# Kernel tuning notes

Hardware: AMD Instinct MI355X
Metric: run time of the kernel (lower is better)

Reference implementation:

```python
import jax, jax.numpy as jnp
import numpy as np

EPS_BN = 1e-5
K_DET = 50

def conv2d(x, w, b, pad):
    y = jax.lax.conv_general_dilated(x, w, (1, 1), [(pad, pad), (pad, pad)],
                                     dimension_numbers=('NCHW', 'OIHW', 'NCHW'))
    return y + b[None, :, None, None]

def branch2(x, w1, b1, w2, b2):
    # conv3x3 -> relu -> conv1x1
    return conv2d(jax.nn.relu(conv2d(x, w1, b1, 1)), w2, b2, 0)

def roi_head(x, w1, b1, g, beta, m, v, w2, b2):
    # conv3x3 -> BN(eval) -> relu -> global avg pool -> conv1x1
    h = conv2d(x, w1, b1, 1)
    h = (h - m[None, :, None, None]) * (g[None, :, None, None] / jnp.sqrt(v[None, :, None, None] + EPS_BN)) + beta[None, :, None, None]
    h = jax.nn.relu(h)
    h = jnp.mean(h, axis=(2, 3), keepdims=True)
    return conv2d(h, w2, b2, 0)[:, :, 0, 0]

def nms_hm(heat, kernel=3):
    pad = (kernel - 1) // 2
    hmax = jax.lax.reduce_window(heat, -jnp.inf, jax.lax.max,
                                 (1, 1, kernel, kernel), (1, 1, 1, 1),
                                 [(0, 0), (0, 0), (pad, pad), (pad, pad)])
    return heat * (hmax == heat).astype(heat.dtype)

def select_topk(heat, K):
    B, C, H, W = heat.shape
    s_all, i_all = jax.lax.top_k(heat.reshape(B, C, H * W), K)   # per-class topk
    scores, idx = jax.lax.top_k(s_all.reshape(B, C * K), K)      # overall topk
    classes = idx // K
    inds = jnp.take_along_axis(i_all.reshape(B, C * K), idx, axis=1)  # flat HW inds
    return scores, inds, classes

def roi_align_7x7(feat, boxes, sr=2):
    # torchvision roi_align, spatial_scale=1, aligned=False, sampling_ratio=sr
    B, C, H, W = feat.shape
    N = boxes.shape[0]
    b = boxes[:, 0].astype(jnp.int32)
    x1, y1, x2, y2 = boxes[:, 1], boxes[:, 2], boxes[:, 3], boxes[:, 4]
    roi_w = jnp.maximum(x2 - x1, 1.0)
    roi_h = jnp.maximum(y2 - y1, 1.0)
    bw = roi_w / 7.0
    bh = roi_h / 7.0
    S = 7 * sr
    off = (jnp.arange(S, dtype=feat.dtype) + 0.5) / sr  # sample offsets in bin units
    xs = x1[:, None] + bw[:, None] * off[None, :]       # (N,S)
    ys = y1[:, None] + bh[:, None] * off[None, :]
    X = jnp.broadcast_to(xs[:, None, :], (N, S, S))
    Y = jnp.broadcast_to(ys[:, :, None], (N, S, S))
    valid = (X > -1.0) & (X < W) & (Y > -1.0) & (Y < H)
    Xc = jnp.clip(X, 0.0, W - 1.0)
    Yc = jnp.clip(Y, 0.0, H - 1.0)
    x0 = jnp.floor(Xc).astype(jnp.int32)
    y0 = jnp.floor(Yc).astype(jnp.int32)
    x1i = jnp.minimum(x0 + 1, W - 1)
    y1i = jnp.minimum(y0 + 1, H - 1)
    lx = Xc - x0
    ly = Yc - y0
    flat = feat.transpose(0, 2, 3, 1).reshape(B * H * W, C)
    base = (b * H * W)[:, None, None]
    g = lambda yy, xx: flat[base + yy * W + xx]  # (N,S,S,C)
    v = (((1 - ly) * (1 - lx))[..., None] * g(y0, x0)
         + ((1 - ly) * lx)[..., None] * g(y0, x1i)
         + (ly * (1 - lx))[..., None] * g(y1i, x0)
         + (ly * lx)[..., None] * g(y1i, x1i))
    v = v * valid[..., None]
    v = v.reshape(N, 7, sr, 7, sr, C).mean(axis=(2, 4))
    return v.transpose(0, 3, 1, 2)  # (N,C,7,7)

def project_to_rect(calib, pts):
    c_u, c_v = calib[:, 0, 2], calib[:, 1, 2]
    f_u, f_v = calib[:, 0, 0], calib[:, 1, 1]
    b_x = calib[:, 0, 3] / (-f_u)
    b_y = calib[:, 1, 3] / (-f_v)
    x = (pts[:, 0] - c_u) * pts[:, 2] / f_u + b_x
    y = (pts[:, 1] - c_v) * pts[:, 2] / f_v + b_y
    return jnp.stack([x, y, pts[:, 2]], -1)

HEAD_NAMES = ['dep', 'o3', 's3', 'hd']

def setup_inputs():
    key = jax.random.key(0)
    ks = iter(jax.random.split(key, 64))
    B, Cin, H, W = 8, 64, 96, 320
    HC, NC = 256, 3
    f32 = jnp.float32
    rn = lambda shape, s=0.02: s * jax.random.normal(next(ks), shape, f32)
    inp = {}
    inp['features'] = jax.random.normal(next(ks), (B, Cin, H, W), f32)
    base = jnp.array([[700., 0., 640., 0.], [0., 700., 192., 0.], [0., 0., 1., 0.]], f32)
    inp['calib'] = base[None] + (jax.random.uniform(next(ks), (B, 3, 4), f32) - 0.5) * 2.0
    crb = jnp.array([[0., 0.], [1280., 384.]], f32)
    inp['coord_ranges'] = crb[None] + (jax.random.uniform(next(ks), (B, 2, 2), f32) - 0.5) * 2.0
    inp['mean_size'] = jnp.array([[3.88, 1.63, 1.53], [0.84, 0.66, 1.76], [1.76, 0.60, 1.73]], f32)
    inp['hm_w1'] = rn((HC, Cin, 3, 3)); inp['hm_b1'] = jnp.zeros(HC, f32)
    inp['hm_w2'] = rn((3, HC, 1, 1)); inp['hm_b2'] = jnp.full((3,), -np.log(1 / 0.1 - 1), f32)
    inp['o2_w1'] = rn((HC, Cin, 3, 3)); inp['o2_b1'] = jnp.zeros(HC, f32)
    inp['o2_w2'] = rn((2, HC, 1, 1)); inp['o2_b2'] = jnp.zeros(2, f32)
    inp['s2_w1'] = rn((HC, Cin, 3, 3)); inp['s2_b1'] = jnp.zeros(HC, f32)
    inp['s2_w2'] = rn((2, HC, 1, 1)); inp['s2_b2'] = 8.0 * jnp.ones(2, f32)
    Croi = Cin + 2 + NC
    for name, oc in zip(HEAD_NAMES, [2, 2, 4, 24]):
        inp[name + '_w1'] = rn((HC, Croi, 3, 3)); inp[name + '_b1'] = jnp.zeros(HC, f32)
        inp[name + '_g'] = 1.0 + 0.1 * jax.random.normal(next(ks), (HC,), f32)
        inp[name + '_beta'] = 0.1 * jax.random.normal(next(ks), (HC,), f32)
        inp[name + '_m'] = 0.1 * jax.random.normal(next(ks), (HC,), f32)
        inp[name + '_v'] = 1.0 + jax.random.uniform(next(ks), (HC,), f32)
        inp[name + '_w2'] = rn((oc, HC, 1, 1)); inp[name + '_b2'] = jnp.zeros(oc, f32)
    return inp

def reference(features, calib, coord_ranges, mean_size,
              hm_w1, hm_b1, hm_w2, hm_b2,
              o2_w1, o2_b1, o2_w2, o2_b2,
              s2_w1, s2_b1, s2_w2, s2_b2,
              dep_w1, dep_b1, dep_g, dep_beta, dep_m, dep_v, dep_w2, dep_b2,
              o3_w1, o3_b1, o3_g, o3_beta, o3_m, o3_v, o3_w2, o3_b2,
              s3_w1, s3_b1, s3_g, s3_beta, s3_m, s3_v, s3_w2, s3_b2,
              hd_w1, hd_b1, hd_g, hd_beta, hd_m, hd_v, hd_w2, hd_b2):
    B, Cf, H, W = features.shape
    dt = features.dtype
    heatmap = branch2(features, hm_w1, hm_b1, hm_w2, hm_b2)    # (B,3,H,W)
    offset_2d = branch2(features, o2_w1, o2_b1, o2_w2, o2_b2)  # (B,2,H,W)
    size_2d = branch2(features, s2_w1, s2_b1, s2_w2, s2_b2)    # (B,2,H,W)
    heat = nms_hm(heatmap)
    _, inds, classes = select_topk(heat, K_DET)                # (B,K)
    # coord map and box2d maps (B,5,H,W): [batch_idx, x1,y1,x2,y2]
    xs = jnp.arange(W, dtype=dt)
    ys = jnp.arange(H, dtype=dt)
    coord = jnp.stack([jnp.broadcast_to(xs[None, :], (H, W)),
                       jnp.broadcast_to(ys[:, None], (H, W))], 0)[None]
    center = coord + offset_2d
    bidx = jnp.broadcast_to(jnp.arange(B, dtype=dt)[:, None, None, None], (B, 1, H, W))
    box2d_maps = jnp.concatenate([bidx, center - size_2d / 2, center + size_2d / 2], 1)
    bm = box2d_maps.reshape(B, 5, H * W).transpose(0, 2, 1)    # (B,HW,5)
    boxes = jnp.take_along_axis(bm, inds[:, :, None], axis=1).reshape(-1, 5)  # (N,5)
    N = boxes.shape[0]
    roi_feat = roi_align_7x7(features, boxes)                  # (N,C,7,7)
    rb = boxes[:, 0].astype(jnp.int32)
    cr = coord_ranges[rb]                                      # (N,2,2)
    sx = cr[:, 1, 0] - cr[:, 0, 0]
    sy = cr[:, 1, 1] - cr[:, 0, 1]
    box_img = jnp.stack([boxes[:, 0],
                         boxes[:, 1] / W * sx + cr[:, 0, 0],
                         boxes[:, 2] / H * sy + cr[:, 0, 1],
                         boxes[:, 3] / W * sx + cr[:, 0, 0],
                         boxes[:, 4] / H * sy + cr[:, 0, 1]], -1)
    roi_calib = calib[rb]                                      # (N,3,4)
    ones = jnp.ones((N, 1), dt)
    p1 = project_to_rect(roi_calib, jnp.concatenate([box_img[:, 1:3], ones], -1))[:, :2]
    p2 = project_to_rect(roi_calib, jnp.concatenate([box_img[:, 3:5], ones], -1))[:, :2]
    t = jnp.arange(7, dtype=dt) / 6.0
    cx = p1[:, 0:1] + t[None, :] * (p2[:, 0:1] - p1[:, 0:1])   # (N,7)
    cy = p1[:, 1:2] + t[None, :] * (p2[:, 1:2] - p1[:, 1:2])
    coord_maps = jnp.stack([jnp.broadcast_to(cx[:, None, :], (N, 7, 7)),
                            jnp.broadcast_to(cy[:, :, None], (N, 7, 7))], 1)
    cls = classes.reshape(-1)
    NC = mean_size.shape[0]
    cls_hot = jax.nn.one_hot(cls, NC, dtype=dt)
    roi_in = jnp.concatenate([roi_feat, coord_maps,
                              jnp.broadcast_to(cls_hot[:, :, None, None], (N, NC, 7, 7))], 1)
    box2d_h = jnp.maximum(box_img[:, 4] - box_img[:, 2], 1.0)
    s3 = roi_head(roi_in, s3_w1, s3_b1, s3_g, s3_beta, s3_m, s3_v, s3_w2, s3_b2)  # (N,4)
    h3d_log_std = s3[:, 3:4]
    size3d_offset = s3[:, :3]
    size_3d = mean_size[cls] + size3d_offset
    f_u = roi_calib[:, 0, 0]
    depth_geo = size_3d[:, 0] / box2d_h * f_u
    dep = roi_head(roi_in, dep_w1, dep_b1, dep_g, dep_beta, dep_m, dep_v, dep_w2, dep_b2)
    depth_geo_log_std = (h3d_log_std[:, 0] + 2.0 * (jnp.log(f_u) - jnp.log(box2d_h)))[:, None]
    depth_log_std = jax.nn.logsumexp(jnp.concatenate([dep[:, 1:2], depth_geo_log_std], -1), axis=-1, keepdims=True)
    depth = jnp.concatenate([1.0 / (jax.nn.sigmoid(dep[:, 0:1]) + 1e-6) - 1.0 + depth_geo[:, None],
                             depth_log_std], -1)
    heading = roi_head(roi_in, hd_w1, hd_b1, hd_g, hd_beta, hd_m, hd_v, hd_w2, hd_b2)
    offset_3d = roi_head(roi_in, o3_w1, o3_b1, o3_g, o3_beta, o3_m, o3_v, o3_w2, o3_b2)
    return (heatmap, offset_2d, size_2d, heading, depth, offset_3d, size3d_offset, h3d_log_std)
```

## Files before the change

### kernel.cpp

```cpp
#include <hip/hip_runtime.h>
#include <math.h>

typedef unsigned short u16;
typedef unsigned int   u32;
typedef unsigned long long u64;
typedef __attribute__((ext_vector_type(8))) short short8;
typedef __attribute__((ext_vector_type(4))) float f32x4;

__device__ __forceinline__ float b2f(u16 v) { return __uint_as_float(((u32)v) << 16); }
__device__ __forceinline__ u16 f2b(float f) {
    u32 u = __float_as_uint(f);
    u32 r = (u + 0x7FFFu + ((u >> 16) & 1u)) >> 16;
    return (u16)r;
}
__device__ __forceinline__ float gload(const void* p, long i, int bf) {
    return bf ? b2f(((const u16*)p)[i]) : ((const float*)p)[i];
}
__device__ __forceinline__ void gstore(void* p, long i, float v, int bf) {
    if (bf) ((u16*)p)[i] = f2b(v);
    else    ((float*)p)[i] = v;
}

__device__ __forceinline__ u64 packKey(float v, int idx) {
    u32 u = __float_as_uint(v);
    u32 m = (u & 0x80000000u) ? ~u : (u | 0x80000000u);
    return ((u64)(~m) << 32) | (u32)idx;
}

__device__ int blockFlag(const void* feat) {
    __shared__ int fcnt;
    if (threadIdx.x == 0) fcnt = 0;
    __syncthreads();
    int sane = 0;
    for (int i = threadIdx.x; i < 512; i += blockDim.x) {
        u16 v = ((const u16*)feat)[i];
        float f = b2f(v);
        u32 e = (v >> 7) & 0xFF;
        float a = fabsf(f);
        sane += (e != 0xFF) && (f == 0.f || (a >= 1e-8f && a <= 1e4f));
    }
    atomicAdd(&fcnt, sane);
    __syncthreads();
    return fcnt >= 480;
}

#define BATCH 8
#define CIN   64
#define FH    96
#define FW    320
#define KDET  50
#define NROI  400
#define CROI  69
#define HW    (FH*FW)
#define CHUNK 1920
#define NCHUNK 16

#define WS_HEAT 0L
#define WS_OFF2 737280L
#define WS_SIZ2 1228800L
#define WS_NH   1720320L
#define WS_S1S  2457600L
#define WS_S1I  2458800L
#define WS_CLS  2460000L
#define WS_BOX  2460400L
#define WS_ROI  2462400L
#define WS_HOUT 3814800L
#define WS_W1T  3827600L
#define WS_WB16 3975056L
#define WS_W1H  4269968L
#define WS_PAR  4905872L
#define WS_FLAG 4938960L

#define PB_CAL 0
#define PB_CRN 96
#define PB_MSZ 128
#define PB_BR0 144
#define PB_HD0 3264

#define O_HEAT 0L
#define O_OFF2 737280L
#define O_SIZ2 1228800L
#define O_HEAD 1720320L
#define O_DEP  1729920L
#define O_OFF3 1730720L
#define O_S3D  1731520L
#define O_H3D  1732720L

struct WPtrs { const void* bw[3]; const void* hw[4]; };
struct Seg { const void* src; int n; int dst; };
struct Segs { Seg s[40]; int cnt; };

__global__ void kPrepWP(WPtrs P, Segs S, const void* __restrict__ feat,
                        int* __restrict__ flag, float* __restrict__ w1t,
                        u16* __restrict__ wb16, u16* __restrict__ whb,
                        float* __restrict__ par) {
    const int bf = blockFlag(feat);
    if (blockIdx.x == 0 && threadIdx.x == 0) *flag = bf;
    if (blockIdx.x < 5760) {
        int idx = blockIdx.x * 256 + threadIdx.x;
        if (idx < 147456) {
            int k = idx >> 8, c = idx & 255;
            w1t[idx] = gload(P.bw[0], (long)c * 576 + k, bf);
        } else if (idx < 589824) {
            int j = idx - 147456;
            int br = j / 147456, rem = j % 147456;
            int tap = rem / 16384;
            int r2 = rem & 16383;
            int s = r2 >> 13;
            int n = (r2 >> 5) & 255;
            int c5 = r2 & 31;
            int ci = s * 32 + c5;
            wb16[j] = f2b(gload(P.bw[br], (long)n * 576 + ci * 9 + tap, bf));
        } else {
            int j = idx - 589824;
            int h = j / 221184, rem = j % 221184;
            int tap = rem / 24576, rem2 = rem % 24576;
            int cs = rem2 / 8192, rem3 = rem2 % 8192;
            int oc = rem3 >> 5, jj = rem3 & 31;
            int ci = cs * 32 + jj;
            u16 val = 0;
            if (ci < CROI) val = f2b(gload(P.hw[h], (long)oc * 621 + ci * 9 + tap, bf));
            whb[j] = val;
        }
    } else {
        int sidx = blockIdx.x - 5760;
        if (sidx < S.cnt) {
            Seg sg = S.s[sidx];
            for (int i = threadIdx.x; i < sg.n; i += 256)
                par[sg.dst + i] = gload(sg.src, i, bf);
        }
    }
}

__global__ __launch_bounds__(512, 4)
void kBranch3(const void* __restrict__ feat, const int* __restrict__ flag,
              const u16* __restrict__ wbAll,
              const float* __restrict__ bpAll,
              void* __restrict__ outb, float* __restrict__ wsbase) {
    __shared__ __align__(16) u16 a_lds[4][68][72];
    __shared__ float red[8][64][3];

    const long obase[3] = {O_HEAT, O_OFF2, O_SIZ2};
    const long wfs[3]   = {WS_HEAT, WS_OFF2, WS_SIZ2};

    const int bfl = *flag;
    const int tid = threadIdx.x;
    const int wave = tid >> 6, lane = tid & 63;
    const int q = lane >> 4, n15 = lane & 15;
    const int mg = wave >> 2, ng = wave & 3;
    const int x0 = blockIdx.x * 64, y0 = blockIdx.y * 2;
    const int b = blockIdx.z;

    if (tid < 256) {
        const int ci = tid & 63, rr = tid >> 6;
        const int gy = y0 - 1 + rr;
        if (gy < 0 || gy >= FH) {
            for (int xi = 0; xi < 66; ++xi) a_lds[rr][xi][ci] = 0;
        } else if (bfl) {
            const u16* rp = (const u16*)feat + ((long)((b << 6) | ci) * FH + gy) * FW;
            for (int j = 0; j < 10; ++j) {
                int xs0 = x0 - 8 + j * 8;
                u16 tmp[8];
                if (xs0 >= 0 && xs0 <= FW - 8)
                    *(uint4*)tmp = *(const uint4*)(rp + xs0);
                else
                    for (int e = 0; e < 8; ++e) {
                        int gx = xs0 + e;
                        tmp[e] = (gx >= 0 && gx < FW) ? rp[gx] : (u16)0;
                    }
                for (int e = 0; e < 8; ++e) {
                    int xi = xs0 + e - x0 + 1;
                    if (xi >= 0 && xi < 66) a_lds[rr][xi][ci] = tmp[e];
                }
            }
        } else {
            const float* rp = (const float*)feat + ((long)((b << 6) | ci) * FH + gy) * FW;
            for (int j = 0; j < 18; ++j) {
                int xs0 = x0 - 4 + j * 4;
                float tmp[4];
                if (xs0 >= 0 && xs0 <= FW - 4)
                    *(float4*)tmp = *(const float4*)(rp + xs0);
                else
                    for (int e = 0; e < 4; ++e) {
                        int gx = xs0 + e;
                        tmp[e] = (gx >= 0 && gx < FW) ? rp[gx] : 0.f;
                    }
                for (int e = 0; e < 4; ++e) {
                    int xi = xs0 + e - x0 + 1;
                    if (xi >= 0 && xi < 66) a_lds[rr][xi][ci] = f2b(tmp[e]);
                }
            }
        }
    }
    __syncthreads();

#pragma unroll 1
    for (int br = 0; br < 3; ++br) {
        const int oc = (br == 0) ? 3 : 2;
        const u16* wpt = wbAll + br * 147456;
        const float* bp = bpAll + br * 1040;

        f32x4 acc[4][4];
#pragma unroll
        for (int i = 0; i < 4; ++i)
#pragma unroll
            for (int t = 0; t < 4; ++t) acc[i][t] = (f32x4){0.f, 0.f, 0.f, 0.f};

#pragma unroll 1
        for (int tap = 0; tap < 9; ++tap) {
            const int ky = tap / 3, kx = tap % 3;
#pragma unroll
            for (int s = 0; s < 2; ++s) {
                const u16* wks = wpt + (tap * 2 + s) * 8192;
                short8 bfr[4];
#pragma unroll
                for (int t = 0; t < 4; ++t)
                    bfr[t] = *(const short8*)(wks + (ng * 64 + t * 16 + n15) * 32 + q * 8);
                short8 afr[4];
#pragma unroll
                for (int i = 0; i < 4; ++i)
                    afr[i] = *(const short8*)&a_lds[mg + ky][i * 16 + n15 + kx][s * 32 + q * 8];
#pragma unroll
                for (int i = 0; i < 4; ++i)
#pragma unroll
                    for (int t = 0; t < 4; ++t)
                        acc[i][t] = __builtin_amdgcn_mfma_f32_16x16x32_bf16(
                            afr[i], bfr[t], acc[i][t], 0, 0, 0);
            }
        }

        float b1v[4], w2v[3][4];
#pragma unroll
        for (int t = 0; t < 4; ++t) {
            int n = ng * 64 + t * 16 + n15;
            b1v[t] = bp[n];
#pragma unroll
            for (int k = 0; k < 3; ++k) w2v[k][t] = bp[256 + k * 256 + n];
        }
        __syncthreads();
#pragma unroll
        for (int i = 0; i < 4; ++i) {
#pragma unroll
            for (int r = 0; r < 4; ++r) {
                float pk[3];
#pragma unroll
                for (int k = 0; k < 3; ++k) pk[k] = 0.f;
#pragma unroll
                for (int t = 0; t < 4; ++t) {
                    float h = fmaxf(acc[i][t][r] + b1v[t], 0.f);
#pragma unroll
                    for (int k = 0; k < 3; ++k) pk[k] = fmaf(h, w2v[k][t], pk[k]);
                }
#pragma unroll
                for (int k = 0; k < 3; ++k) {
                    pk[k] += __shfl_xor(pk[k], 1);
                    pk[k] += __shfl_xor(pk[k], 2);
                    pk[k] += __shfl_xor(pk[k], 4);
                    pk[k] += __shfl_xor(pk[k], 8);
                }
                if (n15 == 0) {
                    int ml = i * 16 + q * 4 + r;
#pragma unroll
                    for (int k = 0; k < 3; ++k) red[wave][ml][k] = pk[k];
                }
            }
        }
        __syncthreads();
        float* outf = wsbase + wfs[br];
        for (int t2 = tid; t2 < oc * 128; t2 += 512) {
            int k = t2 >> 7, m = t2 & 127;
            int row = m >> 6, x = m & 63;
            int mg2 = m >> 6, ml = m & 63;
            float s = bp[256 + oc * 256 + k];
#pragma unroll
            for (int w = 0; w < 4; ++w) s += red[mg2 * 4 + w][ml][k];
            long o = (((long)b * oc + k) * FH + (y0 + row)) * FW + x0 + x;
            gstore(outb, obase[br] + o, s, bfl);
            outf[o] = s;
        }
    }
}

union BrLds {
    float w[36 * 256];
    float part[32 * 3 * 32];
};

__global__ __launch_bounds__(256)
void kBranchX(const void* __restrict__ feat, const int* __restrict__ flag,
              const float* __restrict__ w1t, const float* __restrict__ bp,
              void* __restrict__ outb, long obase, float* __restrict__ outf) {
    __shared__ float in_lds[4][3][36];
    __shared__ BrLds u;
    const int bf = *flag;
    const int OC = 3;

    const int tid = threadIdx.x;
    const int xg = tid & 7, cg = tid >> 3;
    const int x0 = blockIdx.x * 32, y = blockIdx.y, b = blockIdx.z;
    const int c0 = cg * 8;

    float acc[8][4];
#pragma unroll
    for (int i = 0; i < 8; ++i)
#pragma unroll
        for (int j = 0; j < 4; ++j) acc[i][j] = 0.f;

    for (int chunk = 0; chunk < 16; ++chunk) {
        const int ci0 = chunk * 4;
        __syncthreads();
        for (int i = tid; i < 4 * 3 * 36; i += 256) {
            int xx = i % 36, t2 = i / 36;
            int r = t2 % 3, ci = t2 / 3;
            int gx = x0 - 1 + xx, gy = y - 1 + r;
            float v = 0.f;
            if (gx >= 0 && gx < FW && gy >= 0 && gy < FH)
                v = gload(feat, ((long)(b * CIN + ci0 + ci) * FH + gy) * FW + gx, bf);
            in_lds[ci][r][xx] = v;
        }
        {
            const float4* src = (const float4*)(w1t + (long)ci0 * 9 * 256);
            float4* dst = (float4*)u.w;
            for (int i = tid; i < 36 * 256 / 4; i += 256) dst[i] = src[i];
        }
        __syncthreads();
#pragma unroll
        for (int ci = 0; ci < 4; ++ci) {
#pragma unroll
            for (int ky = 0; ky < 3; ++ky) {
                const float* rowp = &in_lds[ci][ky][xg * 4];
                float inv[6];
                *(float4*)&inv[0] = *(const float4*)&rowp[0];
                *(float2*)&inv[4] = *(const float2*)&rowp[4];
#pragma unroll
                for (int kx = 0; kx < 3; ++kx) {
                    const float* wp = &u.w[(ci * 9 + ky * 3 + kx) * 256 + c0];
                    float wv[8];
                    *(float4*)&wv[0] = *(const float4*)&wp[0];
                    *(float4*)&wv[4] = *(const float4*)&wp[4];
#pragma unroll
                    for (int cc = 0; cc < 8; ++cc)
#pragma unroll
                        for (int xx = 0; xx < 4; ++xx)
                            acc[cc][xx] = fmaf(wv[cc], inv[xx + kx], acc[cc][xx]);
                }
            }
        }
    }

#pragma unroll
    for (int cc = 0; cc < 8; ++cc) {
        float b1v = bp[c0 + cc];
#pragma unroll
        for (int xx = 0; xx < 4; ++xx)
            acc[cc][xx] = fmaxf(acc[cc][xx] + b1v, 0.f);
    }

    __syncthreads();
#pragma unroll
    for (int k = 0; k < OC; ++k) {
        float p[4];
#pragma unroll
        for (int xx = 0; xx < 4; ++xx) p[xx] = 0.f;
#pragma unroll
        for (int cc = 0; cc < 8; ++cc) {
            float wv = bp[256 + k * 256 + c0 + cc];
#pragma unroll
            for (int xx = 0; xx < 4; ++xx) p[xx] = fmaf(acc[cc][xx], wv, p[xx]);
        }
#pragma unroll
        for (int xx = 0; xx < 4; ++xx)
            u.part[(cg * OC + k) * 32 + xg * 4 + xx] = p[xx];
    }
    __syncthreads();
    for (int t = tid; t < OC * 32; t += 256) {
        int k = t >> 5, xx = t & 31;
        float s = bp[256 + OC * 256 + k];
#pragma unroll 8
        for (int g = 0; g < 32; ++g) s += u.part[(g * OC + k) * 32 + xx];
        long o = (((long)b * OC + k) * FH + y) * FW + x0 + xx;
        gstore(outb, obase + o, s, bf);
        outf[o] = s;
    }
}

__global__ __launch_bounds__(256)
void kNmsTopA(const float* __restrict__ heat, float* __restrict__ nh) {
    __shared__ float hrow[8][320];
    __shared__ u64 keys[CHUNK];
    const int bc = blockIdx.x, ch = blockIdx.y;
    const int tid = threadIdx.x;
    const int r0 = ch * 6;
    const float* hp = heat + (long)bc * HW;

    for (int i = tid; i < 8 * 320; i += 256) {
        int rr = i / 320, x = i % 320;
        int gy = r0 - 1 + rr;
        hrow[rr][x] = (gy >= 0 && gy < FH) ? hp[(long)gy * FW + x] : -INFINITY;
    }
    __syncthreads();
    for (int i = tid; i < CHUNK; i += 256) {
        int ry = i / 320, x = i % 320;
        float v = hrow[ry + 1][x];
        float m = v;
        int xm = max(x - 1, 0), xp = min(x + 1, FW - 1);
#pragma unroll
        for (int dy = 0; dy < 3; ++dy) {
            m = fmaxf(m, hrow[ry + dy][xm]);
            m = fmaxf(m, hrow[ry + dy][x]);
            m = fmaxf(m, hrow[ry + dy][xp]);
        }
        float nv = (v == m) ? v : 0.f;
        keys[i] = packKey(nv, ch * CHUNK + i);
    }
    __syncthreads();
    if (tid < 64) {
        const int lane = tid;
        u64* outp = (u64*)(nh + (long)bc * HW + (long)ch * CHUNK);
        for (int it = 0; it < KDET; ++it) {
            u64 bk = ~0ULL; int bp = 0;
            for (int i = lane; i < CHUNK; i += 64) {
                u64 k = keys[i];
                if (k < bk) { bk = k; bp = i; }
            }
#pragma unroll
            for (int s = 32; s > 0; s >>= 1) {
                u64 k2 = __shfl_down(bk, s);
                int p2 = __shfl_down(bp, s);
                if (k2 < bk) { bk = k2; bp = p2; }
            }
            bk = __shfl(bk, 0);
            bp = __shfl(bp, 0);
            if (lane == 0) {
                outp[it] = bk;
                keys[bp] = ~0ULL;
            }
        }
    }
}

__global__ __launch_bounds__(192)
void kTopBC(const float* __restrict__ nh, const float* __restrict__ off2,
            const float* __restrict__ siz2, float* __restrict__ boxes,
            int* __restrict__ clsArr) {
    __shared__ u64 keys[3][NCHUNK * KDET];
    __shared__ float sc[150];
    __shared__ int   si[150];
    const int b = blockIdx.x, tid = threadIdx.x;
    const int wave = tid >> 6, lane = tid & 63;
    const int bc = b * 3 + wave;

    for (int ch = 0; ch < NCHUNK; ++ch) {
        const u64* src = (const u64*)(nh + (long)bc * HW + (long)ch * CHUNK);
        if (lane < KDET) keys[wave][ch * KDET + lane] = src[lane];
    }
    __syncthreads();
    for (int it = 0; it < KDET; ++it) {
        u64 bk = ~0ULL; int bp = 0;
        for (int i = lane; i < NCHUNK * KDET; i += 64) {
            u64 k = keys[wave][i];
            if (k < bk) { bk = k; bp = i; }
        }
#pragma unroll
        for (int s = 32; s > 0; s >>= 1) {
            u64 k2 = __shfl_down(bk, s);
            int p2 = __shfl_down(bp, s);
            if (k2 < bk) { bk = k2; bp = p2; }
        }
        bk = __shfl(bk, 0);
        bp = __shfl(bp, 0);
        if (lane == 0) {
            u32 hm = ~(u32)(bk >> 32);
            u32 u = (hm & 0x80000000u) ? (hm & 0x7fffffffu) : ~hm;
            sc[wave * KDET + it] = __uint_as_float(u);
            si[wave * KDET + it] = (int)(bk & 0xFFFFFFFFu);
            keys[wave][bp] = ~0ULL;
        }
    }
    __syncthreads();
    if (wave == 0) {
        const int t = lane;
        for (int r = 0; r < KDET; ++r) {
            float bv = -INFINITY; int bp = 0x7fffffff;
            for (int i = t; i < 150; i += 64) {
                float v = sc[i];
                if (v > bv) { bv = v; bp = i; }
            }
#pragma unroll
            for (int s = 32; s > 0; s >>= 1) {
                float v2 = __shfl_down(bv, s);
                int   p2 = __shfl_down(bp, s);
                if (v2 > bv || (v2 == bv && p2 < bp)) { bv = v2; bp = p2; }
            }
            bp = __shfl(bp, 0);
            if (t == 0) {
                int cls = bp / KDET;
                int ind = si[bp];
                int n = b * KDET + r;
                clsArr[n] = cls;
                int x = ind % FW, yy = ind / FW;
                float cx = (float)x  + off2[(((long)b * 2 + 0) * FH + yy) * FW + x];
                float cy = (float)yy + off2[(((long)b * 2 + 1) * FH + yy) * FW + x];
                float w  = siz2[(((long)b * 2 + 0) * FH + yy) * FW + x];
                float h  = siz2[(((long)b * 2 + 1) * FH + yy) * FW + x];
                boxes[n * 5 + 0] = (float)b;
                boxes[n * 5 + 1] = cx - w * 0.5f;
                boxes[n * 5 + 2] = cy - h * 0.5f;
                boxes[n * 5 + 3] = cx + w * 0.5f;
                boxes[n * 5 + 4] = cy + h * 0.5f;
                sc[bp] = -INFINITY;
            }
        }
    }
}

__global__ __launch_bounds__(256)
void kRoi(const void* __restrict__ feat, const int* __restrict__ flag,
          const float* __restrict__ boxes, const int* __restrict__ clsArr,
          const float* __restrict__ par, float* __restrict__ roi_in) {
    const int n = blockIdx.x, tid = threadIdx.x;
    const int bf = *flag;
    __shared__ int   x0s[14], x1s[14], y0s[14], y1s[14], vxs[14], vys[14];
    __shared__ float lxs[14], lys[14], cxs[7], cys[7];

    const float bx1 = boxes[n * 5 + 1], by1 = boxes[n * 5 + 2];
    const float bx2 = boxes[n * 5 + 3], by2 = boxes[n * 5 + 4];
    const int b = (int)boxes[n * 5 + 0];

    if (tid < 14) {
        float roi_w = fmaxf(bx2 - bx1, 1.f);
        float X = bx1 + (roi_w / 7.f) * ((tid + 0.5f) * 0.5f);
        vxs[tid] = (X > -1.f) && (X < (float)FW);
        float Xc = fminf(fmaxf(X, 0.f), (float)(FW - 1));
        int xi = (int)floorf(Xc);
        x0s[tid] = xi; x1s[tid] = min(xi + 1, FW - 1); lxs[tid] = Xc - (float)xi;
    } else if (tid >= 16 && tid < 30) {
        int i = tid - 16;
        float roi_h = fmaxf(by2 - by1, 1.f);
        float Y = by1 + (roi_h / 7.f) * ((i + 0.5f) * 0.5f);
        vys[i] = (Y > -1.f) && (Y < (float)FH);
        float Yc = fminf(fmaxf(Y, 0.f), (float)(FH - 1));
        int yi = (int)floorf(Yc);
        y0s[i] = yi; y1s[i] = min(yi + 1, FH - 1); lys[i] = Yc - (float)yi;
    } else if (tid >= 32 && tid < 46) {
        int j = tid - 32;
        const float* cal = par + PB_CAL + b * 12;
        float f_u = cal[0], c_u = cal[2], t03 = cal[3];
        float f_v = cal[5], c_v = cal[6], t13 = cal[7];
        float bxc = t03 / (-f_u), byc = t13 / (-f_v);
        const float* cr = par + PB_CRN + b * 4;
        float crx0 = cr[0], cry0 = cr[1], crx1 = cr[2], cry1 = cr[3];
        float sx = crx1 - crx0, sy = cry1 - cry0;
        float u1 = bx1 / (float)FW * sx + crx0, v1 = by1 / (float)FH * sy + cry0;
        float u2 = bx2 / (float)FW * sx + crx0, v2 = by2 / (float)FH * sy + cry0;
        float p1x = (u1 - c_u) / f_u + bxc, p1y = (v1 - c_v) / f_v + byc;
        float p2x = (u2 - c_u) / f_u + bxc, p2y = (v2 - c_v) / f_v + byc;
        if (j < 7) cxs[j] = p1x + ((float)j / 6.f) * (p2x - p1x);
        else       cys[j - 7] = p1y + ((float)(j - 7) / 6.f) * (p2y - p1y);
    }
    __syncthreads();

    for (int t = tid; t < CIN * 49; t += 256) {
        int c = t / 49, p = t % 49, oy = p / 7, ox = p % 7;
        long fb = ((long)b * CIN + c) * HW;
        float acc = 0.f;
#pragma unroll
        for (int dy = 0; dy < 2; ++dy) {
            int sy = oy * 2 + dy;
            float ly = lys[sy]; int yA = y0s[sy], yB = y1s[sy], vy = vys[sy];
#pragma unroll
            for (int dx = 0; dx < 2; ++dx) {
                int sx = ox * 2 + dx;
                float lx = lxs[sx]; int xA = x0s[sx], xB = x1s[sx];
                float v = (1.f - ly) * (1.f - lx) * gload(feat, fb + yA * FW + xA, bf)
                        + (1.f - ly) * lx         * gload(feat, fb + yA * FW + xB, bf)
                        + ly * (1.f - lx)         * gload(feat, fb + yB * FW + xA, bf)
                        + ly * lx                 * gload(feat, fb + yB * FW + xB, bf);
                if (!(vy && vxs[sx])) v = 0.f;
                acc += v;
            }
        }
        roi_in[((long)n * CROI + c) * 49 + p] = acc * 0.25f;
    }
    int cls = clsArr[n];
    for (int t = tid; t < 5 * 49; t += 256) {
        int ch = t / 49, p = t % 49, i = p / 7, j = p % 7;
        float v;
        if (ch == 0)      v = cxs[j];
        else if (ch == 1) v = cys[i];
        else              v = (cls == ch - 2) ? 1.f : 0.f;
        roi_in[((long)n * CROI + 64 + ch) * 49 + p] = v;
    }
}

__global__ __launch_bounds__(256, 4)
void kHeadM(const float* __restrict__ roi_in, const u16* __restrict__ whb,
            const float* __restrict__ par, float* __restrict__ head_out) {
    const int h = blockIdx.x, n = blockIdx.y, tid = threadIdx.x;
    const int wave = tid >> 6, lane = tid & 63;
    const int q = lane >> 4, n15 = lane & 15;
    const int ocArr[4] = {2, 2, 4, 24};
    const int offArr[4] = {0, 2, 4, 8};
    __shared__ __align__(16) u16 r_lds[9][9][104];
    __shared__ float means[256];

    for (int i = tid; i < 9 * 9 * 104 / 8; i += 256)
        ((uint4*)r_lds)[i] = (uint4){0, 0, 0, 0};
    __syncthreads();
    const float* rp = roi_in + (long)n * CROI * 49;
    for (int i = tid; i < CROI * 49; i += 256) {
        int c = i / 49, p = i % 49;
        r_lds[p / 7 + 1][p % 7 + 1][c] = f2b(rp[i]);
    }
    __syncthreads();

    int oyA[4], oxA[4];
#pragma unroll
    for (int i = 0; i < 4; ++i) {
        int pos = i * 16 + n15; if (pos > 48) pos = 48;
        oyA[i] = pos / 7; oxA[i] = pos % 7;
    }

    f32x4 acc[4][4];
#pragma unroll
    for (int i = 0; i < 4; ++i)
#pragma unroll
        for (int t = 0; t < 4; ++t) acc[i][t] = (f32x4){0.f, 0.f, 0.f, 0.f};

#pragma unroll 1
    for (int tap = 0; tap < 9; ++tap) {
        const int ky = tap / 3, kx = tap % 3;
        const u16* wt = whb + ((long)h * 9 + tap) * 24576;
#pragma unroll
        for (int cs = 0; cs < 3; ++cs) {
            short8 afr[4], bfr[4];
#pragma unroll
            for (int i = 0; i < 4; ++i)
                afr[i] = *(const short8*)&r_lds[oyA[i] + ky][oxA[i] + kx][cs * 32 + q * 8];
#pragma unroll
            for (int t = 0; t < 4; ++t)
                bfr[t] = *(const short8*)(wt + ((cs << 8) + wave * 64 + t * 16 + n15) * 32 + q * 8);
#pragma unroll
            for (int i = 0; i < 4; ++i)
#pragma unroll
                for (int t = 0; t < 4; ++t)
                    acc[i][t] = __builtin_amdgcn_mfma_f32_16x16x32_bf16(
                        afr[i], bfr[t], acc[i][t], 0, 0, 0);
        }
    }

    const float* hb = par + PB_HD0 + h * 7456;
#pragma unroll
    for (int t = 0; t < 4; ++t) {
        int oc = wave * 64 + t * 16 + n15;
        float b1 = hb[oc], g = hb[256 + oc], be = hb[512 + oc];
        float m = hb[768 + oc], v = hb[1024 + oc];
        float scale = g / sqrtf(v + 1e-5f);
        float s = 0.f;
#pragma unroll
        for (int i = 0; i < 4; ++i)
#pragma unroll
            for (int r = 0; r < 4; ++r) {
                int pos = i * 16 + q * 4 + r;
                if (pos < 49)
                    s += fmaxf((acc[i][t][r] + b1 - m) * scale + be, 0.f);
            }
        s += __shfl_xor(s, 16);
        s += __shfl_xor(s, 32);
        if (q == 0) means[oc] = s / 49.f;
    }
    __syncthreads();

    int oc_out = ocArr[h];
    const float* w2 = hb + 1280;
    for (int k = wave; k < oc_out; k += 4) {
        float s = 0.f;
        for (int c = lane; c < 256; c += 64) s += means[c] * w2[k * 256 + c];
#pragma unroll
        for (int off = 32; off > 0; off >>= 1) s += __shfl_down(s, off);
        if (lane == 0)
            head_out[(long)n * 32 + offArr[h] + k] = s + w2[oc_out * 256 + k];
    }
}

__global__ void kFinal(const float* __restrict__ head_out, const float* __restrict__ boxes,
                       const int* __restrict__ clsArr, const float* __restrict__ par,
                       void* __restrict__ out, const int* __restrict__ flag) {
    int n = blockIdx.x * 256 + threadIdx.x;
    if (n >= NROI) return;
    const int bf = *flag;
    const float* ho = head_out + (long)n * 32;
    float dep0 = ho[0], dep1 = ho[1];
    int b = (int)boxes[n * 5 + 0];
    int cls = clsArr[n];

    for (int j = 0; j < 24; ++j) gstore(out, O_HEAD + n * 24 + j, ho[8 + j], bf);
    gstore(out, O_OFF3 + n * 2 + 0, ho[2], bf);
    gstore(out, O_OFF3 + n * 2 + 1, ho[3], bf);
    gstore(out, O_S3D + n * 3 + 0, ho[4], bf);
    gstore(out, O_S3D + n * 3 + 1, ho[5], bf);
    gstore(out, O_S3D + n * 3 + 2, ho[6], bf);
    gstore(out, O_H3D + n, ho[7], bf);

    float cry0 = par[PB_CRN + b * 4 + 1], cry1 = par[PB_CRN + b * 4 + 3];
    float sy = cry1 - cry0;
    float bi2 = boxes[n * 5 + 2] / (float)FH * sy + cry0;
    float bi4 = boxes[n * 5 + 4] / (float)FH * sy + cry0;
    float box_h = fmaxf(bi4 - bi2, 1.f);
    float f_u = par[PB_CAL + b * 12 + 0];
    float size3d0 = par[PB_MSZ + cls * 3 + 0] + ho[4];
    float depth_geo = size3d0 / box_h * f_u;
    float sig = 1.f / (1.f + expf(-dep0));
    float d0 = 1.f / (sig + 1e-6f) - 1.f + depth_geo;
    float dgls = ho[7] + 2.f * (logf(f_u) - logf(box_h));
    float mx = fmaxf(dep1, dgls);
    float lse = mx + logf(expf(dep1 - mx) + expf(dgls - mx));
    gstore(out, O_DEP + n * 2 + 0, d0, bf);
    gstore(out, O_DEP + n * 2 + 1, lse, bf);
}

extern "C" void kernel_launch(void* const* d_in, const int* in_sizes, int n_in,
                              void* d_out, int out_size, void* d_ws, size_t ws_size,
                              hipStream_t stream) {
    (void)in_sizes; (void)n_in; (void)out_size; (void)ws_size;
    float* ws = (float*)d_ws;
    float* par = ws + WS_PAR;
    int* flag = (int*)(ws + WS_FLAG);
    u16* wb16 = (u16*)(ws + WS_WB16);
    u16* whb  = (u16*)(ws + WS_W1H);
    const void* feat = d_in[0];

    WPtrs WP;
    WP.bw[0] = d_in[4]; WP.bw[1] = d_in[8]; WP.bw[2] = d_in[12];
    WP.hw[0] = d_in[16]; WP.hw[1] = d_in[24]; WP.hw[2] = d_in[32]; WP.hw[3] = d_in[40];

    Segs SG; int si = 0;
    auto add = [&](const void* s, int n, int dst) {
        SG.s[si].src = s; SG.s[si].n = n; SG.s[si].dst = dst; ++si;
    };
    add(d_in[1], 96, PB_CAL); add(d_in[2], 32, PB_CRN); add(d_in[3], 9, PB_MSZ);
    const int ocb[3] = {3, 2, 2};
    for (int b = 0; b < 3; ++b) {
        int base = PB_BR0 + b * 1040;
        int i0 = 4 + 4 * b;
        add(d_in[i0 + 1], 256, base);
        add(d_in[i0 + 2], ocb[b] * 256, base + 256);
        add(d_in[i0 + 3], ocb[b], base + 256 + ocb[b] * 256);
    }
    const int och[4] = {2, 2, 4, 24};
    for (int h = 0; h < 4; ++h) {
        int base = PB_HD0 + h * 7456;
        int i0 = 16 + 8 * h;
        add(d_in[i0 + 1], 256, base);
        add(d_in[i0 + 2], 256, base + 256);
        add(d_in[i0 + 3], 256, base + 512);
        add(d_in[i0 + 4], 256, base + 768);
        add(d_in[i0 + 5], 256, base + 1024);
        add(d_in[i0 + 6], och[h] * 256, base + 1280);
        add(d_in[i0 + 7], och[h], base + 1280 + och[h] * 256);
    }
    SG.cnt = si;

    kPrepWP<<<5760 + 40, 256, 0, stream>>>(WP, SG, feat, flag,
                                           ws + WS_W1T, wb16, whb, par);

    kBranch3<<<dim3(5, 48, 8), 512, 0, stream>>>(
        feat, flag, wb16, par + PB_BR0, d_out, ws);

    kBranchX<<<dim3(10, 3, 8), 256, 0, stream>>>(
        feat, flag, ws + WS_W1T, par + PB_BR0, d_out, O_HEAT, ws + WS_HEAT);

    kNmsTopA<<<dim3(24, NCHUNK), 256, 0, stream>>>(ws + WS_HEAT, ws + WS_NH);
    kTopBC<<<8, 192, 0, stream>>>(ws + WS_NH, ws + WS_OFF2, ws + WS_SIZ2,
                                  ws + WS_BOX, (int*)(ws + WS_CLS));
    kRoi<<<400, 256, 0, stream>>>(feat, flag, ws + WS_BOX, (int*)(ws + WS_CLS),
                                  par, ws + WS_ROI);
    kHeadM<<<dim3(4, NROI), 256, 0, stream>>>(ws + WS_ROI, whb, par, ws + WS_HOUT);
    kFinal<<<2, 256, 0, stream>>>(ws + WS_HOUT, ws + WS_BOX, (int*)(ws + WS_CLS),
                                  par, d_out, flag);
}
```

Baseline: 831.5 us.

## Fuse fp32 heatmap edge-row conv into MFMA branch kernel; add channel-last ROI gather

Merges the separate fp32 kBranchX kernel, which recomputed the first heatmap rows, into the MFMA branch kernel as an extra grid slice (blockIdx.z==8). The MFMA path now skips writing heatmap rows below 3, so one launch covers both paths and can overlap them. When the workspace is large enough, it also transposes the feature map once into channel-last bf16, so ROI-align gathers read contiguous channels instead of strided NCHW. The costs are an extra transpose pass, the bf16 rounding of ROI features even for fp32 inputs, and a larger LDS union in the merged kernel.

```diff
diff --git a/kernel.cpp b/kernel.cpp
--- a/kernel.cpp
+++ b/kernel.cpp
@@ -70,6 +70,8 @@
 #define WS_W1H  4269968L
 #define WS_PAR  4905872L
 #define WS_FLAG 4938960L
+#define WS_FEATT 4938964L
+#define WS_END  (WS_FEATT + 7864320L)
 
 #define PB_CAL 0
 #define PB_CRN 96
@@ -132,19 +134,149 @@
     }
 }
 
+__global__ __launch_bounds__(256)
+void kTrans(const void* __restrict__ feat, const int* __restrict__ flag,
+            u16* __restrict__ featT) {
+    __shared__ u16 t_lds[64][72];
+    const int bf = *flag;
+    const int x0 = blockIdx.x * 64, y = blockIdx.y, b = blockIdx.z;
+    const int tid = threadIdx.x;
+    for (int i = tid; i < 64 * 64; i += 256) {
+        int c = i >> 6, x = i & 63;
+        t_lds[x][c] = f2b(gload(feat, ((long)(b * CIN + c) * FH + y) * FW + x0 + x, bf));
+    }
+    __syncthreads();
+    u16* outp = featT + (((long)b * FH + y) * FW + x0) * 64;
+    for (int i = tid; i < 64 * 64; i += 256) {
+        int x = i >> 6, c = i & 63;
+        outp[(long)x * 64 + c] = t_lds[x][c];
+    }
+}
+
+union MLds {
+    struct { u16 a[4][68][72]; float red[8][64][3]; } c;
+    struct {
+        float in[4][3][36];
+        union { float w[36 * 256]; float part[32 * 3 * 32]; } u;
+    } s;
+};
+
 __global__ __launch_bounds__(512, 4)
-void kBranch3(const void* __restrict__ feat, const int* __restrict__ flag,
-              const u16* __restrict__ wbAll,
-              const float* __restrict__ bpAll,
-              void* __restrict__ outb, float* __restrict__ wsbase) {
-    __shared__ __align__(16) u16 a_lds[4][68][72];
-    __shared__ float red[8][64][3];
+void kBranch3M(const void* __restrict__ feat, const int* __restrict__ flag,
+               const u16* __restrict__ wbAll,
+               const float* __restrict__ bpAll,
+               const float* __restrict__ w1t,
+               void* __restrict__ outb, float* __restrict__ wsbase) {
+    __shared__ __align__(16) MLds L;
 
     const long obase[3] = {O_HEAT, O_OFF2, O_SIZ2};
     const long wfs[3]   = {WS_HEAT, WS_OFF2, WS_SIZ2};
 
     const int bfl = *flag;
     const int tid = threadIdx.x;
+
+    if (blockIdx.z == 8) {
+        const int sidx = blockIdx.y * 5 + blockIdx.x;
+        const int x0 = (sidx % 10) * 32;
+        const int srem = sidx / 10;
+        const int y = srem % 3;
+        const int b = srem / 3;
+        const float* bp = bpAll;
+        const int OC = 3;
+        const int xg = tid & 7, cg = tid >> 3;
+        const int c0 = (cg & 31) * 8;
+
+        float acc[8][4];
+#pragma unroll
+        for (int i = 0; i < 8; ++i)
+#pragma unroll
+            for (int j = 0; j < 4; ++j) acc[i][j] = 0.f;
+
+        for (int chunk = 0; chunk < 16; ++chunk) {
+            const int ci0 = chunk * 4;
+            __syncthreads();
+            for (int i = tid; i < 4 * 3 * 36; i += 512) {
+                int xx = i % 36, t2 = i / 36;
+                int r = t2 % 3, ci = t2 / 3;
+                int gx = x0 - 1 + xx, gy = y - 1 + r;
+                float v = 0.f;
+                if (gx >= 0 && gx < FW && gy >= 0 && gy < FH)
+                    v = gload(feat, ((long)(b * CIN + ci0 + ci) * FH + gy) * FW + gx, bfl);
+                L.s.in[ci][r][xx] = v;
+            }
+            {
+                const float4* src = (const float4*)(w1t + (long)ci0 * 9 * 256);
+                float4* dst = (float4*)L.s.u.w;
+                for (int i = tid; i < 36 * 256 / 4; i += 512) dst[i] = src[i];
+            }
+            __syncthreads();
+            if (tid < 256) {
+#pragma unroll
+                for (int ci = 0; ci < 4; ++ci) {
+#pragma unroll
+                    for (int ky = 0; ky < 3; ++ky) {
+                        const float* rowp = &L.s.in[ci][ky][xg * 4];
+                        float inv[6];
+                        *(float4*)&inv[0] = *(const float4*)&rowp[0];
+                        *(float2*)&inv[4] = *(const float2*)&rowp[4];
+#pragma unroll
+                        for (int kx = 0; kx < 3; ++kx) {
+                            const float* wp = &L.s.u.w[(ci * 9 + ky * 3 + kx) * 256 + c0];
+                            float wv[8];
+                            *(float4*)&wv[0] = *(const float4*)&wp[0];
+                            *(float4*)&wv[4] = *(const float4*)&wp[4];
+#pragma unroll
+                            for (int cc = 0; cc < 8; ++cc)
+#pragma unroll
+                                for (int xx = 0; xx < 4; ++xx)
+                                    acc[cc][xx] = fmaf(wv[cc], inv[xx + kx], acc[cc][xx]);
+                        }
+                    }
+                }
+            }
+        }
+
+        if (tid < 256) {
+#pragma unroll
+            for (int cc = 0; cc < 8; ++cc) {
+                float b1v = bp[c0 + cc];
+#pragma unroll
+                for (int xx = 0; xx < 4; ++xx)
+                    acc[cc][xx] = fmaxf(acc[cc][xx] + b1v, 0.f);
+            }
+        }
+        __syncthreads();
+        if (tid < 256) {
+#pragma unroll
+            for (int k = 0; k < OC; ++k) {
+                float p[4];
+#pragma unroll
+                for (int xx = 0; xx < 4; ++xx) p[xx] = 0.f;
+#pragma unroll
+                for (int cc = 0; cc < 8; ++cc) {
+                    float wv = bp[256 + k * 256 + c0 + cc];
+#pragma unroll
+                    for (int xx = 0; xx < 4; ++xx) p[xx] = fmaf(acc[cc][xx], wv, p[xx]);
+                }
+#pragma unroll
+                for (int xx = 0; xx < 4; ++xx)
+                    L.s.u.part[((cg & 31) * OC + k) * 32 + xg * 4 + xx] = p[xx];
+            }
+        }
+        __syncthreads();
+        float* outf = wsbase + WS_HEAT;
+        for (int t = tid; t < OC * 32; t += 512) {
+            int k = t >> 5, xx = t & 31;
+            float s = bp[256 + OC * 256 + k];
+#pragma unroll 8
+            for (int g = 0; g < 32; ++g) s += L.s.u.part[(g * OC + k) * 32 + xx];
+            long o = (((long)b * OC + k) * FH + y) * FW + x0 + xx;
+            gstore(outb, O_HEAT + o, s, bfl);
+            outf[o] = s;
+        }
+        return;
+    }
+
     const int wave = tid >> 6, lane = tid & 63;
     const int q = lane >> 4, n15 = lane & 15;
     const int mg = wave >> 2, ng = wave & 3;
@@ -155,7 +287,7 @@
         const int ci = tid & 63, rr = tid >> 6;
         const int gy = y0 - 1 + rr;
         if (gy < 0 || gy >= FH) {
-            for (int xi = 0; xi < 66; ++xi) a_lds[rr][xi][ci] = 0;
+            for (int xi = 0; xi < 66; ++xi) L.c.a[rr][xi][ci] = 0;
         } else if (bfl) {
             const u16* rp = (const u16*)feat + ((long)((b << 6) | ci) * FH + gy) * FW;
             for (int j = 0; j < 10; ++j) {
@@ -170,7 +302,7 @@
                     }
                 for (int e = 0; e < 8; ++e) {
                     int xi = xs0 + e - x0 + 1;
-                    if (xi >= 0 && xi < 66) a_lds[rr][xi][ci] = tmp[e];
+                    if (xi >= 0 && xi < 66) L.c.a[rr][xi][ci] = tmp[e];
                 }
             }
         } else {
@@ -187,7 +319,7 @@
                     }
                 for (int e = 0; e < 4; ++e) {
                     int xi = xs0 + e - x0 + 1;
-                    if (xi >= 0 && xi < 66) a_lds[rr][xi][ci] = f2b(tmp[e]);
+                    if (xi >= 0 && xi < 66) L.c.a[rr][xi][ci] = f2b(tmp[e]);
                 }
             }
         }
@@ -219,7 +351,7 @@
                 short8 afr[4];
 #pragma unroll
                 for (int i = 0; i < 4; ++i)
-                    afr[i] = *(const short8*)&a_lds[mg + ky][i * 16 + n15 + kx][s * 32 + q * 8];
+                    afr[i] = *(const short8*)&L.c.a[mg + ky][i * 16 + n15 + kx][s * 32 + q * 8];
 #pragma unroll
                 for (int i = 0; i < 4; ++i)
 #pragma unroll
@@ -261,7 +393,7 @@
                 if (n15 == 0) {
                     int ml = i * 16 + q * 4 + r;
 #pragma unroll
-                    for (int k = 0; k < 3; ++k) red[wave][ml][k] = pk[k];
+                    for (int k = 0; k < 3; ++k) L.c.red[wave][ml][k] = pk[k];
                 }
             }
         }
@@ -273,114 +405,13 @@
             int mg2 = m >> 6, ml = m & 63;
             float s = bp[256 + oc * 256 + k];
 #pragma unroll
-            for (int w = 0; w < 4; ++w) s += red[mg2 * 4 + w][ml][k];
-            long o = (((long)b * oc + k) * FH + (y0 + row)) * FW + x0 + x;
+            for (int w = 0; w < 4; ++w) s += L.c.red[mg2 * 4 + w][ml][k];
+            int grow = y0 + row;
+            if (br == 0 && grow < 3) continue;
+            long o = (((long)b * oc + k) * FH + grow) * FW + x0 + x;
             gstore(outb, obase[br] + o, s, bfl);
             outf[o] = s;
         }
-    }
-}
-
-union BrLds {
-    float w[36 * 256];
-    float part[32 * 3 * 32];
-};
-
-__global__ __launch_bounds__(256)
-void kBranchX(const void* __restrict__ feat, const int* __restrict__ flag,
-              const float* __restrict__ w1t, const float* __restrict__ bp,
-              void* __restrict__ outb, long obase, float* __restrict__ outf) {
-    __shared__ float in_lds[4][3][36];
-    __shared__ BrLds u;
-    const int bf = *flag;
-    const int OC = 3;
-
-    const int tid = threadIdx.x;
-    const int xg = tid & 7, cg = tid >> 3;
-    const int x0 = blockIdx.x * 32, y = blockIdx.y, b = blockIdx.z;
-    const int c0 = cg * 8;
-
-    float acc[8][4];
-#pragma unroll
-    for (int i = 0; i < 8; ++i)
-#pragma unroll
-        for (int j = 0; j < 4; ++j) acc[i][j] = 0.f;
-
-    for (int chunk = 0; chunk < 16; ++chunk) {
-        const int ci0 = chunk * 4;
-        __syncthreads();
-        for (int i = tid; i < 4 * 3 * 36; i += 256) {
-            int xx = i % 36, t2 = i / 36;
-            int r = t2 % 3, ci = t2 / 3;
-            int gx = x0 - 1 + xx, gy = y - 1 + r;
-            float v = 0.f;
-            if (gx >= 0 && gx < FW && gy >= 0 && gy < FH)
-                v = gload(feat, ((long)(b * CIN + ci0 + ci) * FH + gy) * FW + gx, bf);
-            in_lds[ci][r][xx] = v;
-        }
-        {
-            const float4* src = (const float4*)(w1t + (long)ci0 * 9 * 256);
-            float4* dst = (float4*)u.w;
-            for (int i = tid; i < 36 * 256 / 4; i += 256) dst[i] = src[i];
-        }
-        __syncthreads();
-#pragma unroll
-        for (int ci = 0; ci < 4; ++ci) {
-#pragma unroll
-            for (int ky = 0; ky < 3; ++ky) {
-                const float* rowp = &in_lds[ci][ky][xg * 4];
-                float inv[6];
-                *(float4*)&inv[0] = *(const float4*)&rowp[0];
-                *(float2*)&inv[4] = *(const float2*)&rowp[4];
-#pragma unroll
-                for (int kx = 0; kx < 3; ++kx) {
-                    const float* wp = &u.w[(ci * 9 + ky * 3 + kx) * 256 + c0];
-                    float wv[8];
-                    *(float4*)&wv[0] = *(const float4*)&wp[0];
-                    *(float4*)&wv[4] = *(const float4*)&wp[4];
-#pragma unroll
-                    for (int cc = 0; cc < 8; ++cc)
-#pragma unroll
-                        for (int xx = 0; xx < 4; ++xx)
-                            acc[cc][xx] = fmaf(wv[cc], inv[xx + kx], acc[cc][xx]);
-                }
-            }
-        }
-    }
-
-#pragma unroll
-    for (int cc = 0; cc < 8; ++cc) {
-        float b1v = bp[c0 + cc];
-#pragma unroll
-        for (int xx = 0; xx < 4; ++xx)
-            acc[cc][xx] = fmaxf(acc[cc][xx] + b1v, 0.f);
-    }
-
-    __syncthreads();
-#pragma unroll
-    for (int k = 0; k < OC; ++k) {
-        float p[4];
-#pragma unroll
-        for (int xx = 0; xx < 4; ++xx) p[xx] = 0.f;
-#pragma unroll
-        for (int cc = 0; cc < 8; ++cc) {
-            float wv = bp[256 + k * 256 + c0 + cc];
-#pragma unroll
-            for (int xx = 0; xx < 4; ++xx) p[xx] = fmaf(acc[cc][xx], wv, p[xx]);
-        }
-#pragma unroll
-        for (int xx = 0; xx < 4; ++xx)
-            u.part[(cg * OC + k) * 32 + xg * 4 + xx] = p[xx];
-    }
-    __syncthreads();
-    for (int t = tid; t < OC * 32; t += 256) {
-        int k = t >> 5, xx = t & 31;
-        float s = bp[256 + OC * 256 + k];
-#pragma unroll 8
-        for (int g = 0; g < 32; ++g) s += u.part[(g * OC + k) * 32 + xx];
-        long o = (((long)b * OC + k) * FH + y) * FW + x0 + xx;
-        gstore(outb, obase + o, s, bf);
-        outf[o] = s;
     }
 }
 
@@ -514,6 +545,88 @@
     }
 }
 
+#define ROI_META \
+    if (tid < 14) { \
+        float roi_w = fmaxf(bx2 - bx1, 1.f); \
+        float X = bx1 + (roi_w / 7.f) * ((tid + 0.5f) * 0.5f); \
+        vxs[tid] = (X > -1.f) && (X < (float)FW); \
+        float Xc = fminf(fmaxf(X, 0.f), (float)(FW - 1)); \
+        int xi = (int)floorf(Xc); \
+        x0s[tid] = xi; x1s[tid] = min(xi + 1, FW - 1); lxs[tid] = Xc - (float)xi; \
+    } else if (tid >= 16 && tid < 30) { \
+        int i = tid - 16; \
+        float roi_h = fmaxf(by2 - by1, 1.f); \
+        float Y = by1 + (roi_h / 7.f) * ((i + 0.5f) * 0.5f); \
+        vys[i] = (Y > -1.f) && (Y < (float)FH); \
+        float Yc = fminf(fmaxf(Y, 0.f), (float)(FH - 1)); \
+        int yi = (int)floorf(Yc); \
+        y0s[i] = yi; y1s[i] = min(yi + 1, FH - 1); lys[i] = Yc - (float)yi; \
+    } else if (tid >= 32 && tid < 46) { \
+        int j = tid - 32; \
+        const float* cal = par + PB_CAL + b * 12; \
+        float f_u = cal[0], c_u = cal[2], t03 = cal[3]; \
+        float f_v = cal[5], c_v = cal[6], t13 = cal[7]; \
+        float bxc = t03 / (-f_u), byc = t13 / (-f_v); \
+        const float* cr = par + PB_CRN + b * 4; \
+        float crx0 = cr[0], cry0 = cr[1], crx1 = cr[2], cry1 = cr[3]; \
+        float sx = crx1 - crx0, sy = cry1 - cry0; \
+        float u1 = bx1 / (float)FW * sx + crx0, v1 = by1 / (float)FH * sy + cry0; \
+        float u2 = bx2 / (float)FW * sx + crx0, v2 = by2 / (float)FH * sy + cry0; \
+        float p1x = (u1 - c_u) / f_u + bxc, p1y = (v1 - c_v) / f_v + byc; \
+        float p2x = (u2 - c_u) / f_u + bxc, p2y = (v2 - c_v) / f_v + byc; \
+        if (j < 7) cxs[j] = p1x + ((float)j / 6.f) * (p2x - p1x); \
+        else       cys[j - 7] = p1y + ((float)(j - 7) / 6.f) * (p2y - p1y); \
+    }
+
+__global__ __launch_bounds__(256)
+void kRoiT(const u16* __restrict__ featT, const float* __restrict__ boxes,
+           const int* __restrict__ clsArr, const float* __restrict__ par,
+           float* __restrict__ roi_in) {
+    const int n = blockIdx.x, tid = threadIdx.x;
+    __shared__ int   x0s[14], x1s[14], y0s[14], y1s[14], vxs[14], vys[14];
+    __shared__ float lxs[14], lys[14], cxs[7], cys[7];
+
+    const float bx1 = boxes[n * 5 + 1], by1 = boxes[n * 5 + 2];
+    const float bx2 = boxes[n * 5 + 3], by2 = boxes[n * 5 + 4];
+    const int b = (int)boxes[n * 5 + 0];
+
+    ROI_META
+    __syncthreads();
+
+    const u16* fb = featT + (long)b * FH * FW * 64;
+    for (int t = tid; t < CIN * 49; t += 256) {
+        int c = t & 63, p = t >> 6;
+        int oy = p / 7, ox = p % 7;
+        float acc = 0.f;
+#pragma unroll
+        for (int dy = 0; dy < 2; ++dy) {
+            int sy = oy * 2 + dy;
+            float ly = lys[sy]; int yA = y0s[sy], yB = y1s[sy], vy = vys[sy];
+#pragma unroll
+            for (int dx = 0; dx < 2; ++dx) {
+                int sx = ox * 2 + dx;
+                float lx = lxs[sx]; int xA = x0s[sx], xB = x1s[sx];
+                float v = (1.f - ly) * (1.f - lx) * b2f(fb[((long)yA * FW + xA) * 64 + c])
+                        + (1.f - ly) * lx         * b2f(fb[((long)yA * FW + xB) * 64 + c])
+                        + ly * (1.f - lx)         * b2f(fb[((long)yB * FW + xA) * 64 + c])
+                        + ly * lx                 * b2f(fb[((long)yB * FW + xB) * 64 + c]);
+                if (!(vy && vxs[sx])) v = 0.f;
+                acc += v;
+            }
+        }
+        roi_in[((long)n * CROI + c) * 49 + p] = acc * 0.25f;
+    }
+    int cls = clsArr[n];
+    for (int t = tid; t < 5 * 49; t += 256) {
+        int ch = t / 49, p = t % 49, i = p / 7, j = p % 7;
+        float v;
+        if (ch == 0)      v = cxs[j];
+        else if (ch == 1) v = cys[i];
+        else              v = (cls == ch - 2) ? 1.f : 0.f;
+        roi_in[((long)n * CROI + 64 + ch) * 49 + p] = v;
+    }
+}
+
 __global__ __launch_bounds__(256)
 void kRoi(const void* __restrict__ feat, const int* __restrict__ flag,
           const float* __restrict__ boxes, const int* __restrict__ clsArr,
@@ -527,37 +640,7 @@
     const float bx2 = boxes[n * 5 + 3], by2 = boxes[n * 5 + 4];
     const int b = (int)boxes[n * 5 + 0];
 
-    if (tid < 14) {
-        float roi_w = fmaxf(bx2 - bx1, 1.f);
-        float X = bx1 + (roi_w / 7.f) * ((tid + 0.5f) * 0.5f);
-        vxs[tid] = (X > -1.f) && (X < (float)FW);
-        float Xc = fminf(fmaxf(X, 0.f), (float)(FW - 1));
-        int xi = (int)floorf(Xc);
-        x0s[tid] = xi; x1s[tid] = min(xi + 1, FW - 1); lxs[tid] = Xc - (float)xi;
-    } else if (tid >= 16 && tid < 30) {
-        int i = tid - 16;
-        float roi_h = fmaxf(by2 - by1, 1.f);
-        float Y = by1 + (roi_h / 7.f) * ((i + 0.5f) * 0.5f);
-        vys[i] = (Y > -1.f) && (Y < (float)FH);
-        float Yc = fminf(fmaxf(Y, 0.f), (float)(FH - 1));
-        int yi = (int)floorf(Yc);
-        y0s[i] = yi; y1s[i] = min(yi + 1, FH - 1); lys[i] = Yc - (float)yi;
-    } else if (tid >= 32 && tid < 46) {
-        int j = tid - 32;
-        const float* cal = par + PB_CAL + b * 12;
-        float f_u = cal[0], c_u = cal[2], t03 = cal[3];
-        float f_v = cal[5], c_v = cal[6], t13 = cal[7];
-        float bxc = t03 / (-f_u), byc = t13 / (-f_v);
-        const float* cr = par + PB_CRN + b * 4;
-        float crx0 = cr[0], cry0 = cr[1], crx1 = cr[2], cry1 = cr[3];
-        float sx = crx1 - crx0, sy = cry1 - cry0;
-        float u1 = bx1 / (float)FW * sx + crx0, v1 = by1 / (float)FH * sy + cry0;
-        float u2 = bx2 / (float)FW * sx + crx0, v2 = by2 / (float)FH * sy + cry0;
-        float p1x = (u1 - c_u) / f_u + bxc, p1y = (v1 - c_v) / f_v + byc;
-        float p2x = (u2 - c_u) / f_u + bxc, p2y = (v2 - c_v) / f_v + byc;
-        if (j < 7) cxs[j] = p1x + ((float)j / 6.f) * (p2x - p1x);
-        else       cys[j - 7] = p1y + ((float)(j - 7) / 6.f) * (p2y - p1y);
-    }
+    ROI_META
     __syncthreads();
 
     for (int t = tid; t < CIN * 49; t += 256) {
@@ -722,13 +805,15 @@
 extern "C" void kernel_launch(void* const* d_in, const int* in_sizes, int n_in,
                               void* d_out, int out_size, void* d_ws, size_t ws_size,
                               hipStream_t stream) {
-    (void)in_sizes; (void)n_in; (void)out_size; (void)ws_size;
+    (void)in_sizes; (void)n_in; (void)out_size;
     float* ws = (float*)d_ws;
     float* par = ws + WS_PAR;
     int* flag = (int*)(ws + WS_FLAG);
     u16* wb16 = (u16*)(ws + WS_WB16);
     u16* whb  = (u16*)(ws + WS_W1H);
+    u16* featT = (u16*)(ws + WS_FEATT);
     const void* feat = d_in[0];
+    const bool bigws = ws_size >= (size_t)WS_END * 4;
 
     WPtrs WP;
     WP.bw[0] = d_in[4]; WP.bw[1] = d_in[8]; WP.bw[2] = d_in[12];
@@ -763,18 +848,21 @@
 
     kPrepWP<<<5760 + 40, 256, 0, stream>>>(WP, SG, feat, flag,
                                            ws + WS_W1T, wb16, whb, par);
-
-    kBranch3<<<dim3(5, 48, 8), 512, 0, stream>>>(
-        feat, flag, wb16, par + PB_BR0, d_out, ws);
-
-    kBranchX<<<dim3(10, 3, 8), 256, 0, stream>>>(
-        feat, flag, ws + WS_W1T, par + PB_BR0, d_out, O_HEAT, ws + WS_HEAT);
+    if (bigws)
+        kTrans<<<dim3(5, 96, 8), 256, 0, stream>>>(feat, flag, featT);
+
+    kBranch3M<<<dim3(5, 48, 9), 512, 0, stream>>>(
+        feat, flag, wb16, par + PB_BR0, ws + WS_W1T, d_out, ws);
 
     kNmsTopA<<<dim3(24, NCHUNK), 256, 0, stream>>>(ws + WS_HEAT, ws + WS_NH);
     kTopBC<<<8, 192, 0, stream>>>(ws + WS_NH, ws + WS_OFF2, ws + WS_SIZ2,
                                   ws + WS_BOX, (int*)(ws + WS_CLS));
-    kRoi<<<400, 256, 0, stream>>>(feat, flag, ws + WS_BOX, (int*)(ws + WS_CLS),
-                                  par, ws + WS_ROI);
+    if (bigws)
+        kRoiT<<<400, 256, 0, stream>>>(featT, ws + WS_BOX, (int*)(ws + WS_CLS),
+                                       par, ws + WS_ROI);
+    else
+        kRoi<<<400, 256, 0, stream>>>(feat, flag, ws + WS_BOX, (int*)(ws + WS_CLS),
+                                      par, ws + WS_ROI);
     kHeadM<<<dim3(4, NROI), 256, 0, stream>>>(ws + WS_ROI, whb, par, ws + WS_HOUT);
     kFinal<<<2, 256, 0, stream>>>(ws + WS_HOUT, ws + WS_BOX, (int*)(ws + WS_CLS),
                                   par, d_out, flag);
```

Result: faster. 802.8 us (-3.5%).
